# Performance work log

Hardware: AMD Instinct MI355X
Metric: run time of the kernel (lower is better)

## Reference

```python
import jax, jax.numpy as jnp
import numpy as np

D = 256; HEADS = 8; HD = D // HEADS; LAYERS = 2
GS = 64; K = GS * GS; T = 4; P = 9; R = P // 2
B = 4; N = 511; H = 128; W = 128
SCALE = HD ** -0.5; SIGMA = 0.08


def _ln(x, g, b):
    m = jnp.mean(x, axis=-1, keepdims=True)
    v = jnp.var(x, axis=-1, keepdims=True)
    return (x - m) * jax.lax.rsqrt(v + 1e-5) * g + b


def _gelu(x):
    return jax.nn.gelu(x, approximate=False)  # torch nn.GELU default = exact erf


def _grid_xy():
    c = (jnp.arange(GS, dtype=jnp.float32) + 0.5) / GS
    gy, gx = jnp.meshgrid(c, c, indexing='ij')
    return jnp.stack([gx, gy], axis=-1).reshape(K, 2)  # (K,2)


def _patches(city, meas_xy):
    # city: (B,H,W), meas_xy: (B,N,2) -> (B,N,P,P)
    x = jnp.clip(jnp.round(meas_xy[..., 0] * (W - 1)).astype(jnp.int32), 0, W - 1)
    y = jnp.clip(jnp.round(meas_xy[..., 1] * (H - 1)).astype(jnp.int32), 0, H - 1)
    cp = jnp.pad(city, ((0, 0), (R, R), (R, R)))
    off = jnp.arange(P)  # = (-R..R) + R after padding
    yy = y[:, :, None, None] + off[None, None, :, None]
    xx = x[:, :, None, None] + off[None, None, None, :]
    bi = jnp.arange(B)[:, None, None, None]
    return cp[bi, yy, xx]


def _forward(meas_xy, meas_v, bs_xy, city, meas_W, meas_b, patch_W1, patch_b1,
             patch_W2, patch_b2, bs_W, bs_b, task_emb, taskp_W, taskp_b, grid_pos,
             lnq_g, lnq_b, lnkv_g, lnkv_b, qW, qb, kW, kb, vW, vb, oW, ob,
             dist_raw, dens_raw, lnf_g, lnf_b, f1W, f1b, f2W, f2b,
             tfp_W, tfp_b, head_W, head_b, task_id):
    # measurement tokens
    meas_in = jnp.concatenate([meas_xy, meas_v[..., None]], axis=-1)  # (B,N,3)
    meas_tok = meas_in @ meas_W + meas_b
    pf = _patches(city, meas_xy).reshape(B, N, P * P)
    pf = _gelu(pf @ patch_W1 + patch_b1) @ patch_W2 + patch_b2
    meas_tok = meas_tok + pf
    bs_tok = bs_xy @ bs_W + bs_b  # (B,1,D)
    src = jnp.concatenate([meas_tok, bs_tok], axis=1)          # (B,S,D)
    src_xy = jnp.concatenate([meas_xy, bs_xy], axis=1)         # (B,S,2)
    S = src.shape[1]

    gxy = _grid_xy()
    diff = gxy[None, :, None, :] - src_xy[:, None, :, :]       # (B,K,S,2)
    attn_bias = -jnp.sqrt(jnp.sum(diff * diff, axis=-1))       # (B,K,S)
    dm = gxy[None, :, None, :] - meas_xy[:, None, :, :]        # (B,K,N,2)
    density = jnp.mean(jnp.exp(-jnp.sum(dm * dm, axis=-1) / (2.0 * SIGMA * SIGMA)), axis=-1)  # (B,K)

    task_vec = (task_emb[task_id] @ taskp_W + taskp_b)[:, None, :]
    grid = grid_pos[None] + task_vec                           # (B,K,D)

    for i in range(LAYERS):
        q_in = _ln(grid, lnq_g[i], lnq_b[i])
        kv_in = _ln(src, lnkv_g[i], lnkv_b[i])
        q = (q_in @ qW[i] + qb[i]).reshape(B, K, HEADS, HD)
        k = (kv_in @ kW[i] + kb[i]).reshape(B, S, HEADS, HD)
        v = (kv_in @ vW[i] + vb[i]).reshape(B, S, HEADS, HD)
        scores = jnp.einsum('bkhd,bshd->bhks', q, k) * SCALE   # (B,H,K,S)
        scores = scores + jax.nn.softplus(dist_raw[i]) * attn_bias[:, None]
        gate = 1.0 + jnp.tanh(dens_raw[i]) * density[:, None, :, None]
        attn = jax.nn.softmax(scores * gate, axis=-1)
        out = jnp.einsum('bhks,bshd->bkhd', attn, v).reshape(B, K, D)
        grid = grid + out @ oW[i] + ob[i]
        hid = _ln(grid, lnf_g[i], lnf_b[i])
        grid = grid + _gelu(hid @ f1W[i] + f1b[i]) @ f2W[i] + f2b[i]

    tw = tfp_W[task_id]                                        # (B,D,D)
    tb = tfp_b[task_id]                                        # (B,D)
    tf = _gelu(jnp.einsum('bkd,bdh->bkh', grid, tw) + tb[:, None, :])
    logits = (tf @ head_W + head_b)[..., 0].reshape(B, GS, GS)
    return logits


def setup_inputs() -> dict:
    key = jax.random.key(0)
    ks = iter(jax.random.split(key, 48))
    def nrm(shape, s=0.02):
        return jax.random.normal(next(ks), shape, jnp.float32) * s
    inp = dict(
        meas_xy=jax.random.uniform(next(ks), (B, N, 2), jnp.float32),
        meas_v=jax.random.uniform(next(ks), (B, N), jnp.float32),
        bs_xy=jax.random.uniform(next(ks), (B, 1, 2), jnp.float32),
        city=jax.random.uniform(next(ks), (B, H, W), jnp.float32),
        meas_W=nrm((3, D)), meas_b=jnp.zeros(D),
        patch_W1=nrm((P * P, D)), patch_b1=jnp.zeros(D),
        patch_W2=nrm((D, D)), patch_b2=jnp.zeros(D),
        bs_W=nrm((2, D)), bs_b=jnp.zeros(D),
        task_emb=nrm((T, D), 1.0), taskp_W=nrm((D, D)), taskp_b=jnp.zeros(D),
        grid_pos=nrm((K, D)),
        lnq_g=jnp.ones((LAYERS, D)), lnq_b=jnp.zeros((LAYERS, D)),
        lnkv_g=jnp.ones((LAYERS, D)), lnkv_b=jnp.zeros((LAYERS, D)),
        qW=nrm((LAYERS, D, D)), qb=jnp.zeros((LAYERS, D)),
        kW=nrm((LAYERS, D, D)), kb=jnp.zeros((LAYERS, D)),
        vW=nrm((LAYERS, D, D)), vb=jnp.zeros((LAYERS, D)),
        oW=nrm((LAYERS, D, D)), ob=jnp.zeros((LAYERS, D)),
        dist_raw=nrm((LAYERS,), 0.5), dens_raw=nrm((LAYERS,), 0.5),
        lnf_g=jnp.ones((LAYERS, D)), lnf_b=jnp.zeros((LAYERS, D)),
        f1W=nrm((LAYERS, D, 2 * D)), f1b=jnp.zeros((LAYERS, 2 * D)),
        f2W=nrm((LAYERS, 2 * D, D)), f2b=jnp.zeros((LAYERS, D)),
        tfp_W=nrm((T, D, D)), tfp_b=jnp.zeros((T, D)),
        head_W=nrm((D, 1)), head_b=jnp.zeros(1),
        task_id=jax.random.randint(next(ks), (B,), 0, T),
    )
    return inp


def reference(meas_xy, meas_v, bs_xy, city, meas_W, meas_b, patch_W1, patch_b1,
              patch_W2, patch_b2, bs_W, bs_b, task_emb, taskp_W, taskp_b, grid_pos,
              lnq_g, lnq_b, lnkv_g, lnkv_b, qW, qb, kW, kb, vW, vb, oW, ob,
              dist_raw, dens_raw, lnf_g, lnf_b, f1W, f1b, f2W, f2b,
              tfp_W, tfp_b, head_W, head_b, task_id):
    return _forward(meas_xy, meas_v, bs_xy, city, meas_W, meas_b, patch_W1, patch_b1,
                    patch_W2, patch_b2, bs_W, bs_b, task_emb, taskp_W, taskp_b, grid_pos,
                    lnq_g, lnq_b, lnkv_g, lnkv_b, qW, qb, kW, kb, vW, vb, oW, ob,
                    dist_raw, dens_raw, lnf_g, lnf_b, f1W, f1b, f2W, f2b,
                    tfp_W, tfp_b, head_W, head_b, task_id)
```

## Files before the change

kernel.cpp:

```cpp
#include <hip/hip_runtime.h>
#include <hip/hip_fp16.h>
#include <math.h>

#define DD 256
#define NHEADS 8
#define HDIM 32
#define NLAYERS 2
#define GSZ 64
#define KGRID 4096
#define TTASK 4
#define BB 4
#define NMEAS 511
#define SSRC 512
#define HCITY 128
#define WCITY 128
#define ATT_SCALE 0.17677669529663687f
#define INV2S2 78.125f

typedef unsigned short u16;
typedef __attribute__((ext_vector_type(8))) short short8;
typedef __attribute__((ext_vector_type(4))) float f32x4;

__device__ __forceinline__ u16 f2bf(float f) {
    union { float f; unsigned int u; } x; x.f = f;
    return (u16)((x.u + 0x7fffu + ((x.u >> 16) & 1u)) >> 16);
}
__device__ __forceinline__ unsigned int cvtpk_bf16(float a, float b) {
    unsigned int r;
    asm("v_cvt_pk_bf16_f32 %0, %1, %2" : "=v"(r) : "v"(a), "v"(b));
    return r;
}
__device__ __forceinline__ float h2f(unsigned int u) {
    float r;
    asm("v_cvt_f32_f16 %0, %1" : "=v"(r) : "v"(u));
    return r;
}
__device__ __forceinline__ float gelu_f(float x) {
    return 0.5f * x * (1.0f + erff(x * 0.7071067811865476f));
}
__device__ __forceinline__ void gload16(const u16* g, u16* l) {
    __builtin_amdgcn_global_load_lds(
        (__attribute__((address_space(1))) void*)g,
        (__attribute__((address_space(3))) void*)l, 16, 0, 0);
}

__global__ void task_vec_kernel(const float* __restrict__ task_emb,
                                const float* __restrict__ tpW,
                                const float* __restrict__ tpb,
                                const int* __restrict__ task_id,
                                float* __restrict__ tv) {
    int b = blockIdx.x, t = threadIdx.x;
    int id = task_id[b];
    float a = tpb[t];
    for (int e = 0; e < DD; e++) a = fmaf(task_emb[id * DD + e], tpW[e * DD + t], a);
    tv[b * DD + t] = a;
}

__global__ void grid_init_kernel(const float* __restrict__ grid_pos,
                                 const float* __restrict__ tv,
                                 float* __restrict__ g) {
    int f = blockIdx.x * 256 + threadIdx.x;
    int b = f >> 18;
    float4 gp = ((const float4*)grid_pos)[f & 262143];
    float4 tvv = ((const float4*)tv)[b * 64 + (f & 63)];
    float4 o; o.x = gp.x + tvv.x; o.y = gp.y + tvv.y; o.z = gp.z + tvv.z; o.w = gp.w + tvv.w;
    ((float4*)g)[f] = o;
}

__global__ __launch_bounds__(256) void src_build_kernel(
    const float* __restrict__ meas_xy, const float* __restrict__ meas_v,
    const float* __restrict__ bs_xy, const float* __restrict__ city,
    const float* __restrict__ meas_W, const float* __restrict__ meas_b,
    const float* __restrict__ pW1, const float* __restrict__ pb1,
    const float* __restrict__ pW2, const float* __restrict__ pb2,
    const float* __restrict__ bs_W, const float* __restrict__ bs_b,
    float* __restrict__ src, float* __restrict__ src_xy) {
    __shared__ float sp[81];
    __shared__ float sh[DD];
    int b = blockIdx.x / SSRC, s = blockIdx.x % SSRC, t = threadIdx.x;
    if (s < NMEAS) {
        float mx = meas_xy[(b * NMEAS + s) * 2];
        float my = meas_xy[(b * NMEAS + s) * 2 + 1];
        float mv = meas_v[b * NMEAS + s];
        int cx = (int)rintf(mx * 127.0f); cx = min(max(cx, 0), 127);
        int cy = (int)rintf(my * 127.0f); cy = min(max(cy, 0), 127);
        if (t < 81) {
            int rr = cy + t / 9 - 4, cc = cx + t % 9 - 4;
            sp[t] = (rr >= 0 && rr < HCITY && cc >= 0 && cc < WCITY)
                        ? city[(b * HCITY + rr) * WCITY + cc] : 0.0f;
        }
        __syncthreads();
        float a1 = pb1[t];
        #pragma unroll 9
        for (int e = 0; e < 81; e++) a1 = fmaf(sp[e], pW1[e * DD + t], a1);
        sh[t] = gelu_f(a1);
        __syncthreads();
        float a2 = pb2[t];
        for (int e = 0; e < DD; e++) a2 = fmaf(sh[e], pW2[e * DD + t], a2);
        float mt = mx * meas_W[t] + my * meas_W[DD + t] + mv * meas_W[2 * DD + t] + meas_b[t];
        src[((size_t)(b * SSRC + s)) * DD + t] = mt + a2;
        if (t == 0) { src_xy[(b * SSRC + s) * 2] = mx; src_xy[(b * SSRC + s) * 2 + 1] = my; }
    } else {
        float bx = bs_xy[b * 2], by = bs_xy[b * 2 + 1];
        src[((size_t)(b * SSRC + s)) * DD + t] = bx * bs_W[t] + by * bs_W[DD + t] + bs_b[t];
        if (t == 0) { src_xy[(b * SSRC + s) * 2] = bx; src_xy[(b * SSRC + s) * 2 + 1] = by; }
    }
}

__global__ void density_kernel(const float* __restrict__ meas_xy, float* __restrict__ dens) {
    int w = threadIdx.x >> 6, lane = threadIdx.x & 63;
    int idx = blockIdx.x * 4 + w;
    int b = idx >> 12, k = idx & 4095;
    float gx = ((k & 63) + 0.5f) * (1.0f / 64.0f);
    float gy = ((k >> 6) + 0.5f) * (1.0f / 64.0f);
    float s = 0.0f;
    for (int n = lane; n < NMEAS; n += 64) {
        float2 xy = ((const float2*)meas_xy)[b * NMEAS + n];
        float dx = gx - xy.x, dy = gy - xy.y;
        s += __expf(-(dx * dx + dy * dy) * INV2S2);
    }
    #pragma unroll
    for (int o = 1; o < 64; o <<= 1) s += __shfl_xor(s, o, 64);
    if (lane == 0) dens[idx] = s * (1.0f / 511.0f);
}

__global__ __launch_bounds__(256) void dist_kernel(const float* __restrict__ sxy_g,
                                                   u16* __restrict__ dt) {
    __shared__ float2 sxy[SSRC];
    int bk = blockIdx.x;
    int b = bk >> 12, k = bk & 4095;
    int t = threadIdx.x;
    sxy[t]       = ((const float2*)sxy_g)[b * SSRC + t];
    sxy[t + 256] = ((const float2*)sxy_g)[b * SSRC + t + 256];
    __syncthreads();
    float gx = ((k & 63) + 0.5f) * (1.0f / 64.0f);
    float gy = ((k >> 6) + 0.5f) * (1.0f / 64.0f);
    float2 p0 = sxy[2 * t], p1 = sxy[2 * t + 1];
    float dx0 = gx - p0.x, dy0 = gy - p0.y;
    float dx1 = gx - p1.x, dy1 = gy - p1.y;
    float d0 = sqrtf(dx0 * dx0 + dy0 * dy0);
    float d1 = sqrtf(dx1 * dx1 + dy1 * dy1);
    __half h0 = __float2half(d0), h1 = __float2half(d1);
    unsigned int pk = (unsigned int)__half_as_ushort(h0) |
                      ((unsigned int)__half_as_ushort(h1) << 16);
    ((unsigned int*)dt)[(size_t)bk * 256 + t] = pk;
}

__global__ void ln_kernel(const float* __restrict__ X, const float* __restrict__ g,
                          const float* __restrict__ bvec, u16* __restrict__ Yb, int rows) {
    int w = threadIdx.x >> 6, lane = threadIdx.x & 63;
    int row = blockIdx.x * 4 + w;
    if (row >= rows) return;
    float4 x = ((const float4*)X)[(size_t)row * 64 + lane];
    float s = x.x + x.y + x.z + x.w;
    float q = x.x * x.x + x.y * x.y + x.z * x.z + x.w * x.w;
    #pragma unroll
    for (int o = 1; o < 64; o <<= 1) { s += __shfl_xor(s, o, 64); q += __shfl_xor(q, o, 64); }
    float m = s * (1.0f / 256.0f);
    float v = q * (1.0f / 256.0f) - m * m;
    float rs = rsqrtf(v + 1e-5f);
    float4 gg = ((const float4*)g)[lane], bb = ((const float4*)bvec)[lane];
    float4 y;
    y.x = (x.x - m) * rs * gg.x + bb.x;
    y.y = (x.y - m) * rs * gg.y + bb.y;
    y.z = (x.z - m) * rs * gg.z + bb.z;
    y.w = (x.w - m) * rs * gg.w + bb.w;
    uint2 o2;
    o2.x = cvtpk_bf16(y.x, y.y);
    o2.y = cvtpk_bf16(y.z, y.w);
    *(uint2*)&Yb[(size_t)row * 256 + lane * 4] = o2;
}

__global__ __launch_bounds__(256) void wconv_kernel(const float* __restrict__ W,
                                                    u16* __restrict__ Wt, int Kd, int Nd) {
    __shared__ float L[32][33];
    int z = blockIdx.z;
    size_t zoff = (size_t)z * Kd * Nd;
    int n0 = blockIdx.x * 32, k0 = blockIdx.y * 32;
    int tx = threadIdx.x, ty = threadIdx.y;
    #pragma unroll
    for (int yy = 0; yy < 4; yy++)
        L[tx][ty + 8 * yy] = W[zoff + (size_t)(k0 + ty + 8 * yy) * Nd + n0 + tx];
    __syncthreads();
    #pragma unroll
    for (int yy = 0; yy < 4; yy++)
        Wt[zoff + (size_t)(n0 + ty + 8 * yy) * Kd + k0 + tx] = f2bf(L[ty + 8 * yy][tx]);
}

__global__ __launch_bounds__(256) void vtrans_kernel(const u16* __restrict__ V,
                                                     u16* __restrict__ Vt) {
    __shared__ u16 L[32][33];
    int b = blockIdx.z;
    int n0 = blockIdx.x * 32, s0 = blockIdx.y * 32;
    int tx = threadIdx.x, ty = threadIdx.y;
    #pragma unroll
    for (int yy = 0; yy < 4; yy++)
        L[tx][ty + 8 * yy] = V[(size_t)(b * SSRC + s0 + ty + 8 * yy) * DD + n0 + tx];
    __syncthreads();
    #pragma unroll
    for (int yy = 0; yy < 4; yy++)
        Vt[(size_t)(b * DD + n0 + ty + 8 * yy) * SSRC + s0 + tx] = L[ty + 8 * yy][tx];
}

template <int ACT, int RES, int OBF, int OF32, int BATW, int KD>
__global__ __launch_bounds__(256) void gemm_glds(
    const u16* __restrict__ A, const u16* __restrict__ Wt,
    const float* __restrict__ bias, float* __restrict__ C, u16* __restrict__ Cb,
    int Nfull, const int* __restrict__ task_id, int wstride, int bstride) {
    __shared__ u16 sA[2][128][32];
    __shared__ u16 sB[2][128][32];
    int t = threadIdx.x;
    int w = t >> 6, lane = t & 63, lq = lane & 15, g = lane >> 4;
    int wr = w >> 1, wc = w & 1;
    int m0 = blockIdx.x * 128, n0 = blockIdx.y * 128;
    const u16* Wp = Wt;
    const float* bp = bias;
    if (BATW) {
        int id = task_id[m0 / KGRID];
        Wp += (size_t)id * wstride;
        bp += (size_t)id * bstride;
    }
    int srow = lane >> 2;
    int scol = (lane & 3) * 8;
    const u16* Ag0 = A  + (size_t)(m0 + w * 32 + srow) * KD + scol;
    const u16* Ag1 = Ag0 + (size_t)16 * KD;
    const u16* Bg0 = Wp + (size_t)(n0 + w * 32 + srow) * KD + scol;
    const u16* Bg1 = Bg0 + (size_t)16 * KD;

    f32x4 acc[4][4];
    #pragma unroll
    for (int fm = 0; fm < 4; fm++)
        #pragma unroll
        for (int fn = 0; fn < 4; fn++) acc[fm][fn] = {0.f, 0.f, 0.f, 0.f};

    const int NKS = KD / 32;
    gload16(Ag0, &sA[0][w * 32][0]);
    gload16(Ag1, &sA[0][w * 32 + 16][0]);
    gload16(Bg0, &sB[0][w * 32][0]);
    gload16(Bg1, &sB[0][w * 32 + 16][0]);
    __syncthreads();

    #pragma unroll
    for (int ks = 0; ks < NKS; ks++) {
        int cur = ks & 1;
        if (ks + 1 < NKS) {
            int ko = (ks + 1) * 32;
            gload16(Ag0 + ko, &sA[cur ^ 1][w * 32][0]);
            gload16(Ag1 + ko, &sA[cur ^ 1][w * 32 + 16][0]);
            gload16(Bg0 + ko, &sB[cur ^ 1][w * 32][0]);
            gload16(Bg1 + ko, &sB[cur ^ 1][w * 32 + 16][0]);
        }
        short8 af[4], bf[4];
        #pragma unroll
        for (int fm = 0; fm < 4; fm++)
            af[fm] = *(const short8*)&sA[cur][wr * 64 + fm * 16 + lq][g * 8];
        #pragma unroll
        for (int fn = 0; fn < 4; fn++)
            bf[fn] = *(const short8*)&sB[cur][wc * 64 + fn * 16 + lq][g * 8];
        #pragma unroll
        for (int fm = 0; fm < 4; fm++)
            #pragma unroll
            for (int fn = 0; fn < 4; fn++)
                acc[fm][fn] = __builtin_amdgcn_mfma_f32_16x16x32_bf16(af[fm], bf[fn], acc[fm][fn], 0, 0, 0);
        __syncthreads();
    }

    #pragma unroll
    for (int fm = 0; fm < 4; fm++) {
        int mbase = m0 + wr * 64 + fm * 16 + 4 * g;
        #pragma unroll
        for (int fn = 0; fn < 4; fn++) {
            int col = n0 + wc * 64 + fn * 16 + lq;
            float bv = bp[col];
            #pragma unroll
            for (int r = 0; r < 4; r++) {
                float o = acc[fm][fn][r] + bv;
                if (ACT) o = gelu_f(o);
                size_t off = (size_t)(mbase + r) * Nfull + col;
                if (RES) o += C[off];
                if (OF32) C[off] = o;
                if (OBF) Cb[off] = f2bf(o);
            }
        }
    }
}

#define DPAD 520
__global__ __launch_bounds__(512) void attn_mfma_kernel(
    const u16* __restrict__ Qb, const u16* __restrict__ Kb, const u16* __restrict__ Vt,
    const u16* __restrict__ distT, const float* __restrict__ dens,
    const float* __restrict__ dist_raw, const float* __restrict__ dens_raw,
    u16* __restrict__ O) {
    __shared__ u16 sD[32][DPAD];
    __shared__ u16 sP[16][512];
    int blk = blockIdx.x;
    int kt = blk & 127, b = blk >> 7;
    int t = threadIdx.x;
    {
        int r = t >> 4, cs = (t & 15) * 32;
        const u16* gp = distT + ((size_t)(b * KGRID) + kt * 32 + r) * SSRC + cs;
        uint4 d0 = *(const uint4*)gp;
        uint4 d1 = *(const uint4*)(gp + 8);
        uint4 d2 = *(const uint4*)(gp + 16);
        uint4 d3 = *(const uint4*)(gp + 24);
        *(uint4*)&sD[r][cs] = d0;
        *(uint4*)&sD[r][cs + 8] = d1;
        *(uint4*)&sD[r][cs + 16] = d2;
        *(uint4*)&sD[r][cs + 24] = d3;
    }
    __syncthreads();

    int w = t >> 6, lane = t & 63, lq = lane & 15, g = lane >> 4;
    int h = w;
    const float LOG2E = 1.4426950408889634f;
    float th = tanhf(dens_raw[0]);
    float c1 = log1pf(__expf(dist_raw[0]));
    float gs[2], gc[2];
    short8 qf[2];
    #pragma unroll
    for (int qc = 0; qc < 2; qc++) {
        int qrow = kt * 32 + qc * 16 + lq;
        float gate = 1.0f + th * dens[b * KGRID + qrow];
        gs[qc] = gate * ATT_SCALE * LOG2E;
        gc[qc] = gate * c1 * LOG2E;
        qf[qc] = *(const short8*)(Qb + (size_t)(b * KGRID + qrow) * DD + h * HDIM + g * 8);
    }
    const u16* kbase = Kb + (size_t)b * SSRC * DD + h * HDIM + g * 8;
    const u16* vbase = Vt + ((size_t)(b * NHEADS + h) * HDIM + lq) * SSRC + g * 8;

    f32x4 accA[2] = {{0.f, 0.f, 0.f, 0.f}, {0.f, 0.f, 0.f, 0.f}};
    f32x4 accB[2] = {{0.f, 0.f, 0.f, 0.f}, {0.f, 0.f, 0.f, 0.f}};
    f32x4 zero = {0.f, 0.f, 0.f, 0.f};
    float lsum[2] = {0.f, 0.f};

    for (int s0 = 0; s0 < SSRC; s0 += 32) {
        #pragma unroll
        for (int tl = 0; tl < 2; tl++) {
            int sb = s0 + tl * 16;
            short8 kf = *(const short8*)(kbase + (size_t)(sb + lq) * DD);
            #pragma unroll
            for (int qc = 0; qc < 2; qc++) {
                f32x4 c = __builtin_amdgcn_mfma_f32_16x16x32_bf16(kf, qf[qc], zero, 0, 0, 0);
                uint2 dh = *(const uint2*)&sD[qc * 16 + lq][sb + 4 * g];
                float p0 = exp2f(gs[qc] * c[0] - gc[qc] * h2f(dh.x));
                float p1 = exp2f(gs[qc] * c[1] - gc[qc] * h2f(dh.x >> 16));
                float p2 = exp2f(gs[qc] * c[2] - gc[qc] * h2f(dh.y));
                float p3 = exp2f(gs[qc] * c[3] - gc[qc] * h2f(dh.y >> 16));
                lsum[qc] += (p0 + p1) + (p2 + p3);
                int idx = lq * 32 + tl * 16 + 4 * g;
                *(unsigned int*)&sP[w * 2 + qc][idx]     = cvtpk_bf16(p0, p1);
                *(unsigned int*)&sP[w * 2 + qc][idx + 2] = cvtpk_bf16(p2, p3);
            }
        }
        short8 v0 = *(const short8*)(vbase + s0);
        short8 v1 = *(const short8*)(vbase + 16 * SSRC + s0);
        #pragma unroll
        for (int qc = 0; qc < 2; qc++) {
            short8 pf = *(const short8*)&sP[w * 2 + qc][lq * 32 + g * 8];
            accA[qc] = __builtin_amdgcn_mfma_f32_16x16x32_bf16(v0, pf, accA[qc], 0, 0, 0);
            accB[qc] = __builtin_amdgcn_mfma_f32_16x16x32_bf16(v1, pf, accB[qc], 0, 0, 0);
        }
    }

    #pragma unroll
    for (int qc = 0; qc < 2; qc++) {
        float ls = lsum[qc];
        ls += __shfl_xor(ls, 16, 64);
        ls += __shfl_xor(ls, 32, 64);
        float inv = 1.0f / ls;
        int qrow = kt * 32 + qc * 16 + lq;
        u16* op = O + (size_t)(b * KGRID + qrow) * DD + h * HDIM + 4 * g;
        uint2 o0, o1;
        o0.x = cvtpk_bf16(accA[qc][0] * inv, accA[qc][1] * inv);
        o0.y = cvtpk_bf16(accA[qc][2] * inv, accA[qc][3] * inv);
        o1.x = cvtpk_bf16(accB[qc][0] * inv, accB[qc][1] * inv);
        o1.y = cvtpk_bf16(accB[qc][2] * inv, accB[qc][3] * inv);
        *(uint2*)op = o0;
        *(uint2*)(op + 16) = o1;
    }
}

__global__ void head_kernel(const float* __restrict__ tf, const float* __restrict__ hW,
                            const float* __restrict__ hb, float* __restrict__ out) {
    int w = threadIdx.x >> 6, lane = threadIdx.x & 63;
    int idx = blockIdx.x * 4 + w;
    float4 x = ((const float4*)tf)[(size_t)idx * 64 + lane];
    float4 ww = ((const float4*)hW)[lane];
    float s = x.x * ww.x + x.y * ww.y + x.z * ww.z + x.w * ww.w;
    #pragma unroll
    for (int o = 1; o < 64; o <<= 1) s += __shfl_xor(s, o, 64);
    if (lane == 0) out[idx] = s + hb[0];
}

extern "C" void kernel_launch(void* const* d_in, const int* in_sizes, int n_in,
                              void* d_out, int out_size, void* d_ws, size_t ws_size,
                              hipStream_t stream) {
    const float* meas_xy = (const float*)d_in[0];
    const float* meas_v  = (const float*)d_in[1];
    const float* bs_xy   = (const float*)d_in[2];
    const float* city    = (const float*)d_in[3];
    const float* meas_W  = (const float*)d_in[4];
    const float* meas_b  = (const float*)d_in[5];
    const float* pW1     = (const float*)d_in[6];
    const float* pb1     = (const float*)d_in[7];
    const float* pW2     = (const float*)d_in[8];
    const float* pb2     = (const float*)d_in[9];
    const float* bs_W    = (const float*)d_in[10];
    const float* bs_b    = (const float*)d_in[11];
    const float* task_emb= (const float*)d_in[12];
    const float* taskp_W = (const float*)d_in[13];
    const float* taskp_b = (const float*)d_in[14];
    const float* grid_pos= (const float*)d_in[15];
    const float* lnq_g   = (const float*)d_in[16];
    const float* lnq_b   = (const float*)d_in[17];
    const float* lnkv_g  = (const float*)d_in[18];
    const float* lnkv_b  = (const float*)d_in[19];
    const float* qW      = (const float*)d_in[20];
    const float* qb      = (const float*)d_in[21];
    const float* kW      = (const float*)d_in[22];
    const float* kb      = (const float*)d_in[23];
    const float* vW      = (const float*)d_in[24];
    const float* vb      = (const float*)d_in[25];
    const float* oW      = (const float*)d_in[26];
    const float* ob      = (const float*)d_in[27];
    const float* dist_raw= (const float*)d_in[28];
    const float* dens_raw= (const float*)d_in[29];
    const float* lnf_g   = (const float*)d_in[30];
    const float* lnf_b   = (const float*)d_in[31];
    const float* f1W     = (const float*)d_in[32];
    const float* f1b     = (const float*)d_in[33];
    const float* f2W     = (const float*)d_in[34];
    const float* f2b     = (const float*)d_in[35];
    const float* tfp_W   = (const float*)d_in[36];
    const float* tfp_b   = (const float*)d_in[37];
    const float* head_W  = (const float*)d_in[38];
    const float* head_b  = (const float*)d_in[39];
    const int*   task_id = (const int*)d_in[40];

    float* ws = (float*)d_ws;
    float* src   = ws;
    float* gridb = src + 524288;
    float* tmp1  = gridb + 4194304;
    float* sxyb  = tmp1 + 4194304;
    float* densb = sxyb + 4096;
    float* tvec  = densb + 16384;

    u16* distT = (u16*)tmp1;

    u16* wtq  = (u16*)(tvec + 1024);
    u16* wtk  = wtq  + 131072;
    u16* wtv  = wtk  + 131072;
    u16* wto  = wtv  + 131072;
    u16* wtf1 = wto  + 131072;
    u16* wtf2 = wtf1 + 262144;
    u16* wtt  = wtf2 + 262144;
    u16* kvbf = wtt  + 262144;
    u16* lnbf = kvbf + 524288;
    u16* qbf  = lnbf + 4194304;
    u16* kbf  = qbf  + 4194304;
    u16* vbf  = kbf  + 524288;
    u16* vtbf = vbf  + 524288;
    u16* obf  = vtbf + 524288;
    u16* fhbf = obf  + 4194304;

    const dim3 B32x8(32, 8);

    task_vec_kernel<<<BB, 256, 0, stream>>>(task_emb, taskp_W, taskp_b, task_id, tvec);
    grid_init_kernel<<<4096, 256, 0, stream>>>(grid_pos, tvec, gridb);
    src_build_kernel<<<BB * SSRC, 256, 0, stream>>>(meas_xy, meas_v, bs_xy, city,
                                                    meas_W, meas_b, pW1, pb1, pW2, pb2,
                                                    bs_W, bs_b, src, sxyb);
    density_kernel<<<4096, 256, 0, stream>>>(meas_xy, densb);
    dist_kernel<<<BB * KGRID, 256, 0, stream>>>(sxyb, distT);

    wconv_kernel<<<dim3(8, 8, 2), B32x8, 0, stream>>>(qW, wtq, 256, 256);
    wconv_kernel<<<dim3(8, 8, 2), B32x8, 0, stream>>>(kW, wtk, 256, 256);
    wconv_kernel<<<dim3(8, 8, 2), B32x8, 0, stream>>>(vW, wtv, 256, 256);
    wconv_kernel<<<dim3(8, 8, 2), B32x8, 0, stream>>>(oW, wto, 256, 256);
    wconv_kernel<<<dim3(16, 8, 2), B32x8, 0, stream>>>(f1W, wtf1, 256, 512);
    wconv_kernel<<<dim3(8, 16, 2), B32x8, 0, stream>>>(f2W, wtf2, 512, 256);
    wconv_kernel<<<dim3(8, 8, 4), B32x8, 0, stream>>>(tfp_W, wtt, 256, 256);

    for (int i = 0; i < NLAYERS; i++) {
        const int w16 = i * 65536, bso = i * DD;
        ln_kernel<<<512, 256, 0, stream>>>(src, lnkv_g + bso, lnkv_b + bso, kvbf, 2048);
        gemm_glds<0, 0, 1, 0, 0, 256><<<dim3(16, 2), 256, 0, stream>>>(
            kvbf, wtk + w16, kb + bso, tmp1, kbf, 256, nullptr, 0, 0);
        gemm_glds<0, 0, 1, 0, 0, 256><<<dim3(16, 2), 256, 0, stream>>>(
            kvbf, wtv + w16, vb + bso, tmp1, vbf, 256, nullptr, 0, 0);
        vtrans_kernel<<<dim3(8, 16, 4), B32x8, 0, stream>>>(vbf, vtbf);
        ln_kernel<<<4096, 256, 0, stream>>>(gridb, lnq_g + bso, lnq_b + bso, lnbf, 16384);
        gemm_glds<0, 0, 1, 0, 0, 256><<<dim3(128, 2), 256, 0, stream>>>(
            lnbf, wtq + w16, qb + bso, tmp1, qbf, 256, nullptr, 0, 0);
        attn_mfma_kernel<<<BB * (KGRID / 32), 512, 0, stream>>>(
            qbf, kbf, vtbf, distT, densb, dist_raw + i, dens_raw + i, obf);
        gemm_glds<0, 1, 0, 1, 0, 256><<<dim3(128, 2), 256, 0, stream>>>(
            obf, wto + w16, ob + bso, gridb, obf, 256, nullptr, 0, 0);
        ln_kernel<<<4096, 256, 0, stream>>>(gridb, lnf_g + bso, lnf_b + bso, lnbf, 16384);
        gemm_glds<1, 0, 1, 0, 0, 256><<<dim3(128, 4), 256, 0, stream>>>(
            lnbf, wtf1 + i * 131072, f1b + i * 512, tmp1, fhbf, 512, nullptr, 0, 0);
        gemm_glds<0, 1, 1, 1, 0, 512><<<dim3(128, 2), 256, 0, stream>>>(
            fhbf, wtf2 + i * 131072, f2b + bso, gridb, lnbf, 256, nullptr, 0, 0);
    }

    gemm_glds<1, 0, 0, 1, 1, 256><<<dim3(128, 2), 256, 0, stream>>>(
        lnbf, wtt, tfp_b, tmp1, obf, 256, task_id, 65536, 256);
    head_kernel<<<4096, 256, 0, stream>>>(tmp1, head_W, head_b, (float*)d_out);
}
```

Before: 517.4 us.

## Fuse K/V projections, fold attention gate into Q, fuse head into final GEMM

The separate K and V projection GEMMs are merged into one GEMM over a concatenated weight. The per-query density gate and softmax scale are precomputed and applied as a row scale in the Q projection epilogue, so the attention inner loop does one fma per score. The output head is fused into the task-projection GEMM epilogue using a shuffle reduction and atomicAdd into a head-bias-initialised output, which removes the fp32 intermediate write and the head kernel. The P tile in LDS is padded to reduce bank conflicts. In exchange there is an extra params kernel, and the atomicAdd makes the floating-point summation order nondeterministic.

```diff
diff --git a/kernel.cpp b/kernel.cpp
--- a/kernel.cpp
+++ b/kernel.cpp
@@ -16,6 +16,7 @@
 #define WCITY 128
 #define ATT_SCALE 0.17677669529663687f
 #define INV2S2 78.125f
+#define LOG2E 1.4426950408889634f
 
 typedef unsigned short u16;
 typedef __attribute__((ext_vector_type(8))) short short8;
@@ -124,6 +125,25 @@
     if (lane == 0) dens[idx] = s * (1.0f / 511.0f);
 }
 
+__global__ void params_kernel(const float* __restrict__ dens,
+                              const float* __restrict__ dist_raw,
+                              const float* __restrict__ dens_raw,
+                              const float* __restrict__ kb, const float* __restrict__ vb,
+                              const float* __restrict__ hb,
+                              float* __restrict__ gsc, float* __restrict__ gcc,
+                              float* __restrict__ kvb, float* __restrict__ out) {
+    int idx = blockIdx.x * 256 + threadIdx.x;
+    int l = idx >> 14, i = idx & 16383;
+    float gate = 1.0f + tanhf(dens_raw[l]) * dens[i];
+    gsc[idx] = gate * ATT_SCALE * LOG2E;
+    gcc[idx] = gate * log1pf(__expf(dist_raw[l])) * LOG2E;
+    if (idx < 16384) out[idx] = hb[0];
+    if (idx < 1024) {
+        int ll = idx >> 9, c = idx & 511;
+        kvb[idx] = (c < 256) ? kb[ll * 256 + c] : vb[ll * 256 + c - 256];
+    }
+}
+
 __global__ __launch_bounds__(256) void dist_kernel(const float* __restrict__ sxy_g,
                                                    u16* __restrict__ dt) {
     __shared__ float2 sxy[SSRC];
@@ -172,41 +192,45 @@
 }
 
 __global__ __launch_bounds__(256) void wconv_kernel(const float* __restrict__ W,
-                                                    u16* __restrict__ Wt, int Kd, int Nd) {
+                                                    u16* __restrict__ Wt, int Kd, int Nd,
+                                                    int ostride, int noff) {
     __shared__ float L[32][33];
     int z = blockIdx.z;
-    size_t zoff = (size_t)z * Kd * Nd;
+    size_t zin = (size_t)z * Kd * Nd;
     int n0 = blockIdx.x * 32, k0 = blockIdx.y * 32;
     int tx = threadIdx.x, ty = threadIdx.y;
     #pragma unroll
     for (int yy = 0; yy < 4; yy++)
-        L[tx][ty + 8 * yy] = W[zoff + (size_t)(k0 + ty + 8 * yy) * Nd + n0 + tx];
+        L[tx][ty + 8 * yy] = W[zin + (size_t)(k0 + ty + 8 * yy) * Nd + n0 + tx];
     __syncthreads();
     #pragma unroll
     for (int yy = 0; yy < 4; yy++)
-        Wt[zoff + (size_t)(n0 + ty + 8 * yy) * Kd + k0 + tx] = f2bf(L[ty + 8 * yy][tx]);
+        Wt[(size_t)z * ostride + (size_t)(noff + n0 + ty + 8 * yy) * Kd + k0 + tx] =
+            f2bf(L[ty + 8 * yy][tx]);
 }
 
 __global__ __launch_bounds__(256) void vtrans_kernel(const u16* __restrict__ V,
-                                                     u16* __restrict__ Vt) {
+                                                     u16* __restrict__ Vt,
+                                                     int instride, int inoff) {
     __shared__ u16 L[32][33];
     int b = blockIdx.z;
     int n0 = blockIdx.x * 32, s0 = blockIdx.y * 32;
     int tx = threadIdx.x, ty = threadIdx.y;
     #pragma unroll
     for (int yy = 0; yy < 4; yy++)
-        L[tx][ty + 8 * yy] = V[(size_t)(b * SSRC + s0 + ty + 8 * yy) * DD + n0 + tx];
+        L[tx][ty + 8 * yy] = V[(size_t)(b * SSRC + s0 + ty + 8 * yy) * instride + inoff + n0 + tx];
     __syncthreads();
     #pragma unroll
     for (int yy = 0; yy < 4; yy++)
         Vt[(size_t)(b * DD + n0 + ty + 8 * yy) * SSRC + s0 + tx] = L[ty + 8 * yy][tx];
 }
 
-template <int ACT, int RES, int OBF, int OF32, int BATW, int KD>
+template <int ACT, int RES, int OBF, int OF32, int BATW, int RS, int HEAD, int KD>
 __global__ __launch_bounds__(256) void gemm_glds(
     const u16* __restrict__ A, const u16* __restrict__ Wt,
     const float* __restrict__ bias, float* __restrict__ C, u16* __restrict__ Cb,
-    int Nfull, const int* __restrict__ task_id, int wstride, int bstride) {
+    int Nfull, const int* __restrict__ task_id, int wstride, int bstride,
+    const float* __restrict__ rs, const float* __restrict__ hw) {
     __shared__ u16 sA[2][128][32];
     __shared__ u16 sB[2][128][32];
     int t = threadIdx.x;
@@ -265,34 +289,59 @@
         __syncthreads();
     }
 
+    float hWv[4], bv[4];
+    #pragma unroll
+    for (int fn = 0; fn < 4; fn++) {
+        int col = n0 + wc * 64 + fn * 16 + lq;
+        bv[fn] = bp[col];
+        if (HEAD) hWv[fn] = hw[col];
+    }
     #pragma unroll
     for (int fm = 0; fm < 4; fm++) {
         int mbase = m0 + wr * 64 + fm * 16 + 4 * g;
-        #pragma unroll
-        for (int fn = 0; fn < 4; fn++) {
-            int col = n0 + wc * 64 + fn * 16 + lq;
-            float bv = bp[col];
+        if (HEAD) {
             #pragma unroll
             for (int r = 0; r < 4; r++) {
-                float o = acc[fm][fn][r] + bv;
-                if (ACT) o = gelu_f(o);
-                size_t off = (size_t)(mbase + r) * Nfull + col;
-                if (RES) o += C[off];
-                if (OF32) C[off] = o;
-                if (OBF) Cb[off] = f2bf(o);
+                float part = 0.0f;
+                #pragma unroll
+                for (int fn = 0; fn < 4; fn++) {
+                    float o = acc[fm][fn][r] + bv[fn];
+                    if (ACT) o = gelu_f(o);
+                    part = fmaf(o, hWv[fn], part);
+                }
+                part += __shfl_xor(part, 1, 64);
+                part += __shfl_xor(part, 2, 64);
+                part += __shfl_xor(part, 4, 64);
+                part += __shfl_xor(part, 8, 64);
+                if (lq == 0) atomicAdd(&C[mbase + r], part);
+            }
+        } else {
+            #pragma unroll
+            for (int fn = 0; fn < 4; fn++) {
+                int col = n0 + wc * 64 + fn * 16 + lq;
+                #pragma unroll
+                for (int r = 0; r < 4; r++) {
+                    float o = acc[fm][fn][r] + bv[fn];
+                    if (RS) o *= rs[mbase + r];
+                    if (ACT) o = gelu_f(o);
+                    size_t off = (size_t)(mbase + r) * Nfull + col;
+                    if (RES) o += C[off];
+                    if (OF32) C[off] = o;
+                    if (OBF) Cb[off] = f2bf(o);
+                }
             }
         }
     }
 }
 
 #define DPAD 520
+#define PSTR 40
 __global__ __launch_bounds__(512) void attn_mfma_kernel(
-    const u16* __restrict__ Qb, const u16* __restrict__ Kb, const u16* __restrict__ Vt,
-    const u16* __restrict__ distT, const float* __restrict__ dens,
-    const float* __restrict__ dist_raw, const float* __restrict__ dens_raw,
+    const u16* __restrict__ Qb, const u16* __restrict__ KVo, const u16* __restrict__ Vt,
+    const u16* __restrict__ distT, const float* __restrict__ gccL,
     u16* __restrict__ O) {
     __shared__ u16 sD[32][DPAD];
-    __shared__ u16 sP[16][512];
+    __shared__ u16 sP[16][16 * PSTR];
     int blk = blockIdx.x;
     int kt = blk & 127, b = blk >> 7;
     int t = threadIdx.x;
@@ -312,20 +361,15 @@
 
     int w = t >> 6, lane = t & 63, lq = lane & 15, g = lane >> 4;
     int h = w;
-    const float LOG2E = 1.4426950408889634f;
-    float th = tanhf(dens_raw[0]);
-    float c1 = log1pf(__expf(dist_raw[0]));
-    float gs[2], gc[2];
+    float gc[2];
     short8 qf[2];
     #pragma unroll
     for (int qc = 0; qc < 2; qc++) {
         int qrow = kt * 32 + qc * 16 + lq;
-        float gate = 1.0f + th * dens[b * KGRID + qrow];
-        gs[qc] = gate * ATT_SCALE * LOG2E;
-        gc[qc] = gate * c1 * LOG2E;
+        gc[qc] = gccL[b * KGRID + qrow];
         qf[qc] = *(const short8*)(Qb + (size_t)(b * KGRID + qrow) * DD + h * HDIM + g * 8);
     }
-    const u16* kbase = Kb + (size_t)b * SSRC * DD + h * HDIM + g * 8;
+    const u16* kbase = KVo + (size_t)(b * SSRC) * 512 + h * HDIM + g * 8;
     const u16* vbase = Vt + ((size_t)(b * NHEADS + h) * HDIM + lq) * SSRC + g * 8;
 
     f32x4 accA[2] = {{0.f, 0.f, 0.f, 0.f}, {0.f, 0.f, 0.f, 0.f}};
@@ -337,17 +381,17 @@
         #pragma unroll
         for (int tl = 0; tl < 2; tl++) {
             int sb = s0 + tl * 16;
-            short8 kf = *(const short8*)(kbase + (size_t)(sb + lq) * DD);
+            short8 kf = *(const short8*)(kbase + (size_t)(sb + lq) * 512);
             #pragma unroll
             for (int qc = 0; qc < 2; qc++) {
                 f32x4 c = __builtin_amdgcn_mfma_f32_16x16x32_bf16(kf, qf[qc], zero, 0, 0, 0);
                 uint2 dh = *(const uint2*)&sD[qc * 16 + lq][sb + 4 * g];
-                float p0 = exp2f(gs[qc] * c[0] - gc[qc] * h2f(dh.x));
-                float p1 = exp2f(gs[qc] * c[1] - gc[qc] * h2f(dh.x >> 16));
-                float p2 = exp2f(gs[qc] * c[2] - gc[qc] * h2f(dh.y));
-                float p3 = exp2f(gs[qc] * c[3] - gc[qc] * h2f(dh.y >> 16));
+                float p0 = exp2f(fmaf(-gc[qc], h2f(dh.x), c[0]));
+                float p1 = exp2f(fmaf(-gc[qc], h2f(dh.x >> 16), c[1]));
+                float p2 = exp2f(fmaf(-gc[qc], h2f(dh.y), c[2]));
+                float p3 = exp2f(fmaf(-gc[qc], h2f(dh.y >> 16), c[3]));
                 lsum[qc] += (p0 + p1) + (p2 + p3);
-                int idx = lq * 32 + tl * 16 + 4 * g;
+                int idx = lq * PSTR + tl * 16 + 4 * g;
                 *(unsigned int*)&sP[w * 2 + qc][idx]     = cvtpk_bf16(p0, p1);
                 *(unsigned int*)&sP[w * 2 + qc][idx + 2] = cvtpk_bf16(p2, p3);
             }
@@ -356,7 +400,7 @@
         short8 v1 = *(const short8*)(vbase + 16 * SSRC + s0);
         #pragma unroll
         for (int qc = 0; qc < 2; qc++) {
-            short8 pf = *(const short8*)&sP[w * 2 + qc][lq * 32 + g * 8];
+            short8 pf = *(const short8*)&sP[w * 2 + qc][lq * PSTR + g * 8];
             accA[qc] = __builtin_amdgcn_mfma_f32_16x16x32_bf16(v0, pf, accA[qc], 0, 0, 0);
             accB[qc] = __builtin_amdgcn_mfma_f32_16x16x32_bf16(v1, pf, accB[qc], 0, 0, 0);
         }
@@ -378,18 +422,6 @@
         *(uint2*)op = o0;
         *(uint2*)(op + 16) = o1;
     }
-}
-
-__global__ void head_kernel(const float* __restrict__ tf, const float* __restrict__ hW,
-                            const float* __restrict__ hb, float* __restrict__ out) {
-    int w = threadIdx.x >> 6, lane = threadIdx.x & 63;
-    int idx = blockIdx.x * 4 + w;
-    float4 x = ((const float4*)tf)[(size_t)idx * 64 + lane];
-    float4 ww = ((const float4*)hW)[lane];
-    float s = x.x * ww.x + x.y * ww.y + x.z * ww.z + x.w * ww.w;
-    #pragma unroll
-    for (int o = 1; o < 64; o <<= 1) s += __shfl_xor(s, o, 64);
-    if (lane == 0) out[idx] = s + hb[0];
 }
 
 extern "C" void kernel_launch(void* const* d_in, const int* in_sizes, int n_in,
@@ -440,26 +472,27 @@
     float* ws = (float*)d_ws;
     float* src   = ws;
     float* gridb = src + 524288;
-    float* tmp1  = gridb + 4194304;
-    float* sxyb  = tmp1 + 4194304;
+    float* distTf= gridb + 4194304;
+    float* sxyb  = distTf + 4194304;
     float* densb = sxyb + 4096;
     float* tvec  = densb + 16384;
-
-    u16* distT = (u16*)tmp1;
-
-    u16* wtq  = (u16*)(tvec + 1024);
-    u16* wtk  = wtq  + 131072;
-    u16* wtv  = wtk  + 131072;
-    u16* wto  = wtv  + 131072;
-    u16* wtf1 = wto  + 131072;
+    float* gsc   = tvec + 1024;
+    float* gcc   = gsc + 32768;
+    float* kvb   = gcc + 32768;
+
+    u16* distT = (u16*)distTf;
+
+    u16* wtq  = (u16*)(kvb + 1024);
+    u16* wto  = wtq  + 131072;
+    u16* wkv  = wto  + 131072;
+    u16* wtf1 = wkv  + 262144;
     u16* wtf2 = wtf1 + 262144;
     u16* wtt  = wtf2 + 262144;
     u16* kvbf = wtt  + 262144;
     u16* lnbf = kvbf + 524288;
     u16* qbf  = lnbf + 4194304;
-    u16* kbf  = qbf  + 4194304;
-    u16* vbf  = kbf  + 524288;
-    u16* vtbf = vbf  + 524288;
+    u16* kvo  = qbf  + 4194304;
+    u16* vtbf = kvo  + 1048576;
     u16* obf  = vtbf + 524288;
     u16* fhbf = obf  + 4194304;
 
@@ -471,39 +504,38 @@
                                                     meas_W, meas_b, pW1, pb1, pW2, pb2,
                                                     bs_W, bs_b, src, sxyb);
     density_kernel<<<4096, 256, 0, stream>>>(meas_xy, densb);
+    params_kernel<<<128, 256, 0, stream>>>(densb, dist_raw, dens_raw, kb, vb, head_b,
+                                           gsc, gcc, kvb, (float*)d_out);
     dist_kernel<<<BB * KGRID, 256, 0, stream>>>(sxyb, distT);
 
-    wconv_kernel<<<dim3(8, 8, 2), B32x8, 0, stream>>>(qW, wtq, 256, 256);
-    wconv_kernel<<<dim3(8, 8, 2), B32x8, 0, stream>>>(kW, wtk, 256, 256);
-    wconv_kernel<<<dim3(8, 8, 2), B32x8, 0, stream>>>(vW, wtv, 256, 256);
-    wconv_kernel<<<dim3(8, 8, 2), B32x8, 0, stream>>>(oW, wto, 256, 256);
-    wconv_kernel<<<dim3(16, 8, 2), B32x8, 0, stream>>>(f1W, wtf1, 256, 512);
-    wconv_kernel<<<dim3(8, 16, 2), B32x8, 0, stream>>>(f2W, wtf2, 512, 256);
-    wconv_kernel<<<dim3(8, 8, 4), B32x8, 0, stream>>>(tfp_W, wtt, 256, 256);
+    wconv_kernel<<<dim3(8, 8, 2), B32x8, 0, stream>>>(qW, wtq, 256, 256, 65536, 0);
+    wconv_kernel<<<dim3(8, 8, 2), B32x8, 0, stream>>>(kW, wkv, 256, 256, 131072, 0);
+    wconv_kernel<<<dim3(8, 8, 2), B32x8, 0, stream>>>(vW, wkv, 256, 256, 131072, 256);
+    wconv_kernel<<<dim3(8, 8, 2), B32x8, 0, stream>>>(oW, wto, 256, 256, 65536, 0);
+    wconv_kernel<<<dim3(16, 8, 2), B32x8, 0, stream>>>(f1W, wtf1, 256, 512, 131072, 0);
+    wconv_kernel<<<dim3(8, 16, 2), B32x8, 0, stream>>>(f2W, wtf2, 512, 256, 131072, 0);
+    wconv_kernel<<<dim3(8, 8, 4), B32x8, 0, stream>>>(tfp_W, wtt, 256, 256, 65536, 0);
 
     for (int i = 0; i < NLAYERS; i++) {
         const int w16 = i * 65536, bso = i * DD;
         ln_kernel<<<512, 256, 0, stream>>>(src, lnkv_g + bso, lnkv_b + bso, kvbf, 2048);
-        gemm_glds<0, 0, 1, 0, 0, 256><<<dim3(16, 2), 256, 0, stream>>>(
-            kvbf, wtk + w16, kb + bso, tmp1, kbf, 256, nullptr, 0, 0);
-        gemm_glds<0, 0, 1, 0, 0, 256><<<dim3(16, 2), 256, 0, stream>>>(
-            kvbf, wtv + w16, vb + bso, tmp1, vbf, 256, nullptr, 0, 0);
-        vtrans_kernel<<<dim3(8, 16, 4), B32x8, 0, stream>>>(vbf, vtbf);
+        gemm_glds<0, 0, 1, 0, 0, 0, 0, 256><<<dim3(16, 4), 256, 0, stream>>>(
+            kvbf, wkv + i * 131072, kvb + i * 512, nullptr, kvo, 512, nullptr, 0, 0, nullptr, nullptr);
+        vtrans_kernel<<<dim3(8, 16, 4), B32x8, 0, stream>>>(kvo, vtbf, 512, 256);
         ln_kernel<<<4096, 256, 0, stream>>>(gridb, lnq_g + bso, lnq_b + bso, lnbf, 16384);
-        gemm_glds<0, 0, 1, 0, 0, 256><<<dim3(128, 2), 256, 0, stream>>>(
-            lnbf, wtq + w16, qb + bso, tmp1, qbf, 256, nullptr, 0, 0);
+        gemm_glds<0, 0, 1, 0, 0, 1, 0, 256><<<dim3(128, 2), 256, 0, stream>>>(
+            lnbf, wtq + w16, qb + bso, nullptr, qbf, 256, nullptr, 0, 0, gsc + i * 16384, nullptr);
         attn_mfma_kernel<<<BB * (KGRID / 32), 512, 0, stream>>>(
-            qbf, kbf, vtbf, distT, densb, dist_raw + i, dens_raw + i, obf);
-        gemm_glds<0, 1, 0, 1, 0, 256><<<dim3(128, 2), 256, 0, stream>>>(
-            obf, wto + w16, ob + bso, gridb, obf, 256, nullptr, 0, 0);
+            qbf, kvo, vtbf, distT, gcc + i * 16384, obf);
+        gemm_glds<0, 1, 0, 1, 0, 0, 0, 256><<<dim3(128, 2), 256, 0, stream>>>(
+            obf, wto + w16, ob + bso, gridb, obf, 256, nullptr, 0, 0, nullptr, nullptr);
         ln_kernel<<<4096, 256, 0, stream>>>(gridb, lnf_g + bso, lnf_b + bso, lnbf, 16384);
-        gemm_glds<1, 0, 1, 0, 0, 256><<<dim3(128, 4), 256, 0, stream>>>(
-            lnbf, wtf1 + i * 131072, f1b + i * 512, tmp1, fhbf, 512, nullptr, 0, 0);
-        gemm_glds<0, 1, 1, 1, 0, 512><<<dim3(128, 2), 256, 0, stream>>>(
-            fhbf, wtf2 + i * 131072, f2b + bso, gridb, lnbf, 256, nullptr, 0, 0);
-    }
-
-    gemm_glds<1, 0, 0, 1, 1, 256><<<dim3(128, 2), 256, 0, stream>>>(
-        lnbf, wtt, tfp_b, tmp1, obf, 256, task_id, 65536, 256);
-    head_kernel<<<4096, 256, 0, stream>>>(tmp1, head_W, head_b, (float*)d_out);
-}
+        gemm_glds<1, 0, 1, 0, 0, 0, 0, 256><<<dim3(128, 4), 256, 0, stream>>>(
+            lnbf, wtf1 + i * 131072, f1b + i * 512, nullptr, fhbf, 512, nullptr, 0, 0, nullptr, nullptr);
+        gemm_glds<0, 1, 1, 1, 0, 0, 0, 512><<<dim3(128, 2), 256, 0, stream>>>(
+            fhbf, wtf2 + i * 131072, f2b + bso, gridb, lnbf, 256, nullptr, 0, 0, nullptr, nullptr);
+    }
+
+    gemm_glds<1, 0, 0, 0, 1, 0, 1, 256><<<dim3(128, 2), 256, 0, stream>>>(
+        lnbf, wtt, tfp_b, (float*)d_out, nullptr, 256, task_id, 65536, 256, nullptr, head_W);
+}
```

Result: faster. 478.9 us (-7.4%).
